# Optimization experiments

Hardware: AMD Instinct MI355X
Metric: run time of the kernel (lower is better)

The kernel has to match this reference:

```python
import jax, jax.numpy as jnp
import numpy as np

B, S, IN, OUT, L, R = 2, 8192, 2048, 2048, 4, 32


def setup_inputs() -> dict:
    key = jax.random.key(0)
    ks = jax.random.split(key, 6)
    return {
        "x": jax.random.normal(ks[0], (B, S, IN), dtype=jnp.float32),
        "weight": jax.random.normal(ks[1], (OUT, IN), dtype=jnp.float32) * 0.02,
        "bias": jax.random.normal(ks[2], (OUT,), dtype=jnp.float32) * 0.02,
        "downs": jax.random.normal(ks[3], (L, R, IN), dtype=jnp.float32) * 0.02,
        "ups": jax.random.normal(ks[4], (L, OUT, R), dtype=jnp.float32) * 0.02,
        "scales": jax.random.uniform(ks[5], (L,), dtype=jnp.float32),
    }


def reference(x, weight, bias, downs, ups, scales):
    # Base linear: y = x @ W.T + b
    y = jnp.einsum("bsi,oi->bso", x, weight) + bias
    # Low-rank LoRA deltas, grouped across adapters:
    # tmp[b,s,l,r] = x @ down_l.T ; delta = sum_l scale_l * tmp_l @ up_l.T
    tmp = jnp.einsum("bsi,lri->bslr", x, downs)  # [B,S,L,R]
    tmp = tmp * scales[None, None, :, None]       # fold per-adapter scale
    delta = jnp.einsum("bslr,lor->bso", tmp, ups)  # [B,S,OUT]
    return y + delta
```

## Files before the change

kernel.cpp:

```cpp
#include <hip/hip_runtime.h>

#define M_DIM 16384
#define N_DIM 2048
#define K_DIM 2048
#define L_AD 4
#define R_AD 32

typedef __bf16 bf16_t;
typedef bf16_t bf16x8 __attribute__((ext_vector_type(8)));
typedef bf16_t bf16x4 __attribute__((ext_vector_type(4)));
typedef float f32x4 __attribute__((ext_vector_type(4)));

#define BM 128
#define BN 128
#define BK 64

__device__ __forceinline__ void async_load16(const void* g, void* l) {
  __builtin_amdgcn_global_load_lds(
      (const __attribute__((address_space(1))) unsigned int*)g,
      (__attribute__((address_space(3))) unsigned int*)l, 16, 0, 0);
}

__global__ __launch_bounds__(256) void convert_x_kernel(
    const float* __restrict__ X, bf16_t* __restrict__ Xb) {
  const size_t base = ((size_t)blockIdx.x * 256 + threadIdx.x) * 8;
  f32x4 lo = *(const f32x4*)(X + base);
  f32x4 hi = *(const f32x4*)(X + base + 4);
  bf16x8 v;
  v[0] = (bf16_t)lo[0]; v[1] = (bf16_t)lo[1];
  v[2] = (bf16_t)lo[2]; v[3] = (bf16_t)lo[3];
  v[4] = (bf16_t)hi[0]; v[5] = (bf16_t)hi[1];
  v[6] = (bf16_t)hi[2]; v[7] = (bf16_t)hi[3];
  *(bf16x8*)(Xb + base) = v;
}

__global__ __launch_bounds__(256) void build_weff_kernel(
    const float* __restrict__ W, const float* __restrict__ downs,
    const float* __restrict__ ups, const float* __restrict__ scales,
    bf16_t* __restrict__ weff) {
  __shared__ float up_s[64 * 129];
  __shared__ float down_s[128 * 64];
  const int t = threadIdx.x;
  const int n0 = blockIdx.y * 64;
  const int k0 = blockIdx.x * 64;

  for (int l = 0; l < L_AD; ++l) {
    const float sc = scales[l];
    const float* up_l = ups + (size_t)l * N_DIM * R_AD;
    #pragma unroll
    for (int j = 0; j < 8; ++j) {
      int flat = j * 256 + t;
      int nl = flat >> 5, r = flat & 31;
      up_s[nl * 129 + l * 32 + r] = sc * up_l[(size_t)(n0 + nl) * R_AD + r];
    }
  }
  #pragma unroll
  for (int j = 0; j < 32; ++j) {
    int flat = j * 256 + t;
    int lr = flat >> 6, kk = flat & 63;
    down_s[lr * 64 + kk] = downs[(size_t)lr * K_DIM + k0 + kk];
  }
  __syncthreads();

  const int tn = t >> 4, tk = t & 15;
  float acc[4][4] = {};
  for (int lr = 0; lr < L_AD * R_AD; ++lr) {
    f32x4 b = *(const f32x4*)&down_s[lr * 64 + tk * 4];
    #pragma unroll
    for (int u = 0; u < 4; ++u) {
      float a = up_s[(tn * 4 + u) * 129 + lr];
      #pragma unroll
      for (int v = 0; v < 4; ++v) acc[u][v] += a * b[v];
    }
  }
  #pragma unroll
  for (int u = 0; u < 4; ++u) {
    int n = n0 + tn * 4 + u;
    f32x4 wv = *(const f32x4*)&W[(size_t)n * K_DIM + k0 + tk * 4];
    bf16x4 o;
    #pragma unroll
    for (int v = 0; v < 4; ++v) o[v] = (bf16_t)(acc[u][v] + wv[v]);
    *(bf16x4*)&weff[(size_t)n * K_DIM + k0 + tk * 4] = o;
  }
}

#define BARRIER() __builtin_amdgcn_s_barrier()
#define SCHEDB() __builtin_amdgcn_sched_barrier(0)
#define VMCNT4() asm volatile("s_waitcnt vmcnt(4)" ::: "memory")
#define VMCNT0() asm volatile("s_waitcnt vmcnt(0)" ::: "memory")

__global__ __launch_bounds__(512, 2) void gemm_bf16_256(
    const bf16_t* __restrict__ Xb, const bf16_t* __restrict__ Wb,
    const float* __restrict__ bias, float* __restrict__ out) {
  __shared__ __align__(16) bf16_t sm[2][2][16384];

  const int orig = blockIdx.x;
  const int swz = (orig & 7) * 64 + (orig >> 3);
  const int m0 = (swz >> 3) * 256;
  const int n0 = (swz & 7) * 256;

  const int t = threadIdx.x;
  const int l = t & 63;
  const int w = t >> 6;
  const int wm = w >> 2, wn = w & 3;
  const int col = l & 15, quad = l >> 4;

  const int d0 = w * 64 + l;
  const int row0 = d0 >> 3;
  const int c0 = (d0 & 7) ^ (row0 & 7);
  const bf16_t* Ab = Xb + (size_t)(m0 + row0) * K_DIM + c0 * 8;
  const bf16_t* Bb = Wb + (size_t)(n0 + row0) * K_DIM + c0 * 8;

  const int arow = wm * 128 + col;
  const int brow = wn * 64 + col;

  float bn[4];
  #pragma unroll
  for (int g = 0; g < 4; ++g) bn[g] = bias[n0 + wn * 64 + g * 16 + col];

  f32x4 acc[8][4] = {};
  bf16x8 aLo[4][2], aHi[4][2], bB[4][2];

#define STG(Gb, B_, OP, H, KT)                                                 \
  do {                                                                         \
    async_load16((Gb) + ((size_t)(H)*128) * K_DIM + (size_t)(KT)*64,           \
                 &sm[B_][OP][(H)*8192 + d0 * 8]);                              \
    async_load16((Gb) + ((size_t)(H)*128 + 64) * K_DIM + (size_t)(KT)*64,      \
                 &sm[B_][OP][(H)*8192 + (d0 + 512) * 8]);                      \
  } while (0)

#define RDA(dst, fi, F0, B_)                                                   \
  do {                                                                         \
    const int R_ = arow + ((F0) + (fi)) * 16;                                  \
    const int rl_ = R_ & 127, h_ = R_ >> 7;                                    \
    _Pragma("unroll") for (int ks_ = 0; ks_ < 2; ++ks_) {                      \
      const int sl_ = (ks_ * 4 + quad) ^ (rl_ & 7);                            \
      dst[fi][ks_] =                                                           \
          *(const bf16x8*)&sm[B_][0][h_ * 8192 + (rl_ * 8 + sl_) * 8];         \
    }                                                                          \
  } while (0)

#define RDB(gi, B_)                                                            \
  do {                                                                         \
    const int R_ = brow + (gi) * 16;                                           \
    const int rl_ = R_ & 127, h_ = R_ >> 7;                                    \
    _Pragma("unroll") for (int ks_ = 0; ks_ < 2; ++ks_) {                      \
      const int sl_ = (ks_ * 4 + quad) ^ (rl_ & 7);                            \
      bB[gi][ks_] =                                                            \
          *(const bf16x8*)&sm[B_][1][h_ * 8192 + (rl_ * 8 + sl_) * 8];         \
    }                                                                          \
  } while (0)

#define MF(AARR, FA, G0)                                                       \
  do {                                                                         \
    __builtin_amdgcn_s_setprio(1);                                             \
    _Pragma("unroll") for (int f_ = 0; f_ < 4; ++f_)                           \
        _Pragma("unroll") for (int g_ = 0; g_ < 2; ++g_)                       \
            _Pragma("unroll") for (int ks_ = 0; ks_ < 2; ++ks_)                \
                acc[(FA) + f_][(G0) + g_] =                                    \
                    __builtin_amdgcn_mfma_f32_16x16x32_bf16(                   \
                        AARR[f_][ks_], bB[(G0) + g_][ks_],                     \
                        acc[(FA) + f_][(G0) + g_], 0, 0, 0);                   \
    __builtin_amdgcn_s_setprio(0);                                             \
  } while (0)

  STG(Bb, 0, 1, 0, 0); STG(Bb, 0, 1, 1, 0);
  STG(Ab, 0, 0, 0, 0); STG(Ab, 0, 0, 1, 0);
  STG(Bb, 1, 1, 0, 1); STG(Bb, 1, 1, 1, 1);
  VMCNT4();
  BARRIER();

  for (int j = 0; j < 16; ++j) {
    const int k1 = 2 * j + 1;
    const int kt2 = (2 * j + 2 < 32) ? 2 * j + 2 : 31;
    const int kt3 = (2 * j + 3 < 32) ? 2 * j + 3 : 31;

    STG(Ab, 1, 0, 0, k1); SCHEDB();
    RDA(aLo, 0, 0, 0); RDB(0, 0); RDB(1, 0);
    RDA(aLo, 1, 0, 0); RDA(aLo, 2, 0, 0); RDA(aLo, 3, 0, 0);
    SCHEDB();
    RDB(2, 0); RDB(3, 0);
    SCHEDB();
    MF(aLo, 0, 0);
    SCHEDB(); BARRIER();
    STG(Ab, 1, 0, 1, k1); SCHEDB();
    RDA(aHi, 0, 4, 0); RDA(aHi, 1, 4, 0); RDA(aHi, 2, 4, 0); RDA(aHi, 3, 4, 0);
    SCHEDB();
    MF(aLo, 0, 2);
    SCHEDB(); BARRIER();
    STG(Bb, 0, 1, 0, kt2); SCHEDB();
    MF(aHi, 4, 2);
    SCHEDB(); BARRIER();
    STG(Bb, 0, 1, 1, kt2); SCHEDB();
    MF(aHi, 4, 0);
    SCHEDB(); VMCNT4(); BARRIER();
    STG(Ab, 0, 0, 0, kt2); SCHEDB();
    RDA(aLo, 0, 0, 1); RDB(0, 1); RDB(1, 1);
    RDA(aLo, 1, 0, 1); RDA(aLo, 2, 0, 1); RDA(aLo, 3, 0, 1);
    SCHEDB();
    RDB(2, 1); RDB(3, 1);
    SCHEDB();
    MF(aLo, 0, 0);
    SCHEDB(); BARRIER();
    STG(Ab, 0, 0, 1, kt2); SCHEDB();
    RDA(aHi, 0, 4, 1); RDA(aHi, 1, 4, 1); RDA(aHi, 2, 4, 1); RDA(aHi, 3, 4, 1);
    SCHEDB();
    MF(aLo, 0, 2);
    SCHEDB(); BARRIER();
    STG(Bb, 1, 1, 0, kt3); SCHEDB();
    MF(aHi, 4, 2);
    SCHEDB(); BARRIER();
    STG(Bb, 1, 1, 1, kt3); SCHEDB();
    MF(aHi, 4, 0);
    SCHEDB(); VMCNT4(); BARRIER();
  }

  VMCNT0();
  BARRIER();

  #pragma unroll
  for (int f = 0; f < 8; ++f) {
    const int m = m0 + wm * 128 + f * 16 + quad * 4;
    const bf16x8* dummy = 0; (void)dummy;
    #pragma unroll
    for (int g = 0; g < 4; ++g) {
      const int n = n0 + wn * 64 + g * 16 + col;
      float* op = out + (size_t)m * N_DIM + n;
      #pragma unroll
      for (int r = 0; r < 4; ++r) op[(size_t)r * N_DIM] = acc[f][g][r] + bn[g];
    }
  }
#undef STG
#undef RDA
#undef RDB
#undef MF
}

#define SA 72
__global__ __launch_bounds__(256) void lora_gemm_fallback(
    const float* __restrict__ X, const bf16_t* __restrict__ Wb,
    const float* __restrict__ bias, float* __restrict__ out) {
  __shared__ __align__(16) bf16_t As[BM * SA];
  __shared__ __align__(16) bf16_t Bs[BN * BK];

  const int t = threadIdx.x;
  const int lane = t & 63;
  const int wv = t >> 6;
  const int wm = wv >> 1, wn = wv & 1;
  const int col = lane & 15, quad = lane >> 4;
  const int m0 = blockIdx.y * BM;
  const int n0 = blockIdx.x * BN;
  const int srow = t >> 3;
  const int soct = t & 7;

  f32x4 acc[4][4] = {};
  float bn[4];
  #pragma unroll
  for (int j = 0; j < 4; ++j) bn[j] = bias[n0 + wn * 64 + j * 16 + col];

  for (int kt = 0; kt < K_DIM / BK; ++kt) {
    const int kg = kt * BK;
    #pragma unroll
    for (int j = 0; j < 4; ++j) {
      int n = j * 32 + srow;
      int c = soct ^ (n & 7);
      async_load16(Wb + (size_t)(n0 + n) * K_DIM + kg + c * 8,
                   &Bs[(size_t)(j * 256 + t) * 8]);
    }
    #pragma unroll
    for (int j = 0; j < 4; ++j) {
      int m = j * 32 + srow;
      const f32x4* src = (const f32x4*)(X + (size_t)(m0 + m) * K_DIM + kg + soct * 8);
      f32x4 lo = src[0], hi = src[1];
      bf16x8 v;
      v[0] = (bf16_t)lo[0]; v[1] = (bf16_t)lo[1];
      v[2] = (bf16_t)lo[2]; v[3] = (bf16_t)lo[3];
      v[4] = (bf16_t)hi[0]; v[5] = (bf16_t)hi[1];
      v[6] = (bf16_t)hi[2]; v[7] = (bf16_t)hi[3];
      *(bf16x8*)&As[m * SA + soct * 8] = v;
    }
    __syncthreads();

    #pragma unroll
    for (int ks = 0; ks < 2; ++ks) {
      bf16x8 af[4], bfr[4];
      #pragma unroll
      for (int i = 0; i < 4; ++i)
        af[i] = *(const bf16x8*)&As[(wm * 64 + i * 16 + col) * SA + ks * 32 + quad * 8];
      #pragma unroll
      for (int j = 0; j < 4; ++j) {
        int n = wn * 64 + j * 16 + col;
        int p = (ks * 4 + quad) ^ (n & 7);
        bfr[j] = *(const bf16x8*)&Bs[n * BK + p * 8];
      }
      #pragma unroll
      for (int i = 0; i < 4; ++i) {
        #pragma unroll
        for (int j = 0; j < 4; ++j)
          acc[i][j] = __builtin_amdgcn_mfma_f32_16x16x32_bf16(af[i], bfr[j], acc[i][j], 0, 0, 0);
      }
    }
    __syncthreads();
  }

  #pragma unroll
  for (int i = 0; i < 4; ++i) {
    #pragma unroll
    for (int r = 0; r < 4; ++r) {
      int m = m0 + wm * 64 + i * 16 + quad * 4 + r;
      float* orow = out + (size_t)m * N_DIM + n0 + wn * 64 + col;
      #pragma unroll
      for (int j = 0; j < 4; ++j)
        orow[j * 16] = acc[i][j][r] + bn[j];
    }
  }
}

extern "C" void kernel_launch(void* const* d_in, const int* in_sizes, int n_in,
                              void* d_out, int out_size, void* d_ws, size_t ws_size,
                              hipStream_t stream) {
  const float* x      = (const float*)d_in[0];
  const float* weight = (const float*)d_in[1];
  const float* bias   = (const float*)d_in[2];
  const float* downs  = (const float*)d_in[3];
  const float* ups    = (const float*)d_in[4];
  const float* scales = (const float*)d_in[5];
  float* out = (float*)d_out;

  const size_t weff_bytes = (size_t)N_DIM * K_DIM * 2;
  const size_t xb_bytes   = (size_t)M_DIM * K_DIM * 2;
  bf16_t* weff = (bf16_t*)d_ws;

  dim3 g1(K_DIM / 64, N_DIM / 64);
  build_weff_kernel<<<g1, 256, 0, stream>>>(weight, downs, ups, scales, weff);

  if (ws_size >= weff_bytes + xb_bytes) {
    bf16_t* xb = (bf16_t*)((char*)d_ws + weff_bytes);
    const size_t n_elem = (size_t)M_DIM * K_DIM;
    convert_x_kernel<<<(unsigned)(n_elem / (256 * 8)), 256, 0, stream>>>(x, xb);
    gemm_bf16_256<<<dim3((M_DIM / 256) * (N_DIM / 256)), 512, 0, stream>>>(
        xb, weff, bias, out);
  } else {
    dim3 g2(N_DIM / BN, M_DIM / BM);
    lora_gemm_fallback<<<g2, 256, 0, stream>>>(x, weff, bias, out);
  }
}
```

Before: 370.5 us.

## Switch main GEMM to 32x32x16 MFMA with fine-grained lgkmcnt-pipelined phases

Replaces the 16x16x32 bf16 MFMA tiling with 32x32x16 MFMAs, so each wave computes a 128x64 tile as 4x2 blocks of 32x32. LDS fragment reads and their lane mapping are reworked to match. The main loop is split into phases that issue LDS reads, then stage the next global-to-LDS copy, then interleave MFMAs with partial lgkmcnt waits so compute can start before every fragment has arrived. Larger MFMAs need fewer instructions and fewer LDS reads per flop. The costs are a more complex hand schedule with more barriers and a different register footprint.

```diff
diff --git a/kernel.cpp b/kernel.cpp
--- a/kernel.cpp
+++ b/kernel.cpp
@@ -10,6 +10,7 @@
 typedef bf16_t bf16x8 __attribute__((ext_vector_type(8)));
 typedef bf16_t bf16x4 __attribute__((ext_vector_type(4)));
 typedef float f32x4 __attribute__((ext_vector_type(4)));
+typedef float f32x16 __attribute__((ext_vector_type(16)));
 
 #define BM 128
 #define BN 128
@@ -86,6 +87,7 @@
 
 #define BARRIER() __builtin_amdgcn_s_barrier()
 #define SCHEDB() __builtin_amdgcn_sched_barrier(0)
+#define LGKM(N) asm volatile("s_waitcnt lgkmcnt(" #N ")" ::: "memory")
 #define VMCNT4() asm volatile("s_waitcnt vmcnt(4)" ::: "memory")
 #define VMCNT0() asm volatile("s_waitcnt vmcnt(0)" ::: "memory")
 
@@ -103,7 +105,8 @@
   const int l = t & 63;
   const int w = t >> 6;
   const int wm = w >> 2, wn = w & 3;
-  const int col = l & 15, quad = l >> 4;
+  const int l5 = l & 31;
+  const int half = l >> 5;
 
   const int d0 = w * 64 + l;
   const int row0 = d0 >> 3;
@@ -111,15 +114,12 @@
   const bf16_t* Ab = Xb + (size_t)(m0 + row0) * K_DIM + c0 * 8;
   const bf16_t* Bb = Wb + (size_t)(n0 + row0) * K_DIM + c0 * 8;
 
-  const int arow = wm * 128 + col;
-  const int brow = wn * 64 + col;
-
-  float bn[4];
-  #pragma unroll
-  for (int g = 0; g < 4; ++g) bn[g] = bias[n0 + wn * 64 + g * 16 + col];
-
-  f32x4 acc[8][4] = {};
-  bf16x8 aLo[4][2], aHi[4][2], bB[4][2];
+  float bn[2];
+  #pragma unroll
+  for (int g = 0; g < 2; ++g) bn[g] = bias[n0 + wn * 64 + g * 32 + l5];
+
+  f32x16 acc[4][2] = {};
+  bf16x8 aLo[2][4], aHi[2][4], bB[2][4];
 
 #define STG(Gb, B_, OP, H, KT)                                                 \
   do {                                                                         \
@@ -129,39 +129,27 @@
                  &sm[B_][OP][(H)*8192 + (d0 + 512) * 8]);                      \
   } while (0)
 
-#define RDA(dst, fi, F0, B_)                                                   \
+#define RA(dst, fi, F, ks, B_)                                                 \
   do {                                                                         \
-    const int R_ = arow + ((F0) + (fi)) * 16;                                  \
+    const int rl_ = (F)*32 + l5;                                               \
+    const int sl_ = ((ks)*2 + half) ^ (rl_ & 7);                               \
+    dst[fi][ks] = *(const bf16x8*)&sm[B_][0][wm * 8192 + (rl_ * 8 + sl_) * 8]; \
+  } while (0)
+
+#define RB(gi, ks, B_)                                                         \
+  do {                                                                         \
+    const int R_ = wn * 64 + (gi)*32 + l5;                                     \
     const int rl_ = R_ & 127, h_ = R_ >> 7;                                    \
-    _Pragma("unroll") for (int ks_ = 0; ks_ < 2; ++ks_) {                      \
-      const int sl_ = (ks_ * 4 + quad) ^ (rl_ & 7);                            \
-      dst[fi][ks_] =                                                           \
-          *(const bf16x8*)&sm[B_][0][h_ * 8192 + (rl_ * 8 + sl_) * 8];         \
-    }                                                                          \
+    const int sl_ = ((ks)*2 + half) ^ (rl_ & 7);                               \
+    bB[gi][ks] = *(const bf16x8*)&sm[B_][1][h_ * 8192 + (rl_ * 8 + sl_) * 8];  \
   } while (0)
 
-#define RDB(gi, B_)                                                            \
+#define MF2(AARR, FA, G, ks)                                                   \
   do {                                                                         \
-    const int R_ = brow + (gi) * 16;                                           \
-    const int rl_ = R_ & 127, h_ = R_ >> 7;                                    \
-    _Pragma("unroll") for (int ks_ = 0; ks_ < 2; ++ks_) {                      \
-      const int sl_ = (ks_ * 4 + quad) ^ (rl_ & 7);                            \
-      bB[gi][ks_] =                                                            \
-          *(const bf16x8*)&sm[B_][1][h_ * 8192 + (rl_ * 8 + sl_) * 8];         \
-    }                                                                          \
-  } while (0)
-
-#define MF(AARR, FA, G0)                                                       \
-  do {                                                                         \
-    __builtin_amdgcn_s_setprio(1);                                             \
-    _Pragma("unroll") for (int f_ = 0; f_ < 4; ++f_)                           \
-        _Pragma("unroll") for (int g_ = 0; g_ < 2; ++g_)                       \
-            _Pragma("unroll") for (int ks_ = 0; ks_ < 2; ++ks_)                \
-                acc[(FA) + f_][(G0) + g_] =                                    \
-                    __builtin_amdgcn_mfma_f32_16x16x32_bf16(                   \
-                        AARR[f_][ks_], bB[(G0) + g_][ks_],                     \
-                        acc[(FA) + f_][(G0) + g_], 0, 0, 0);                   \
-    __builtin_amdgcn_s_setprio(0);                                             \
+    acc[(FA) + 0][G] = __builtin_amdgcn_mfma_f32_32x32x16_bf16(                \
+        AARR[0][ks], bB[G][ks], acc[(FA) + 0][G], 0, 0, 0);                    \
+    acc[(FA) + 1][G] = __builtin_amdgcn_mfma_f32_32x32x16_bf16(                \
+        AARR[1][ks], bB[G][ks], acc[(FA) + 1][G], 0, 0, 0);                    \
   } while (0)
 
   STG(Bb, 0, 1, 0, 0); STG(Bb, 0, 1, 1, 0);
@@ -175,65 +163,94 @@
     const int kt2 = (2 * j + 2 < 32) ? 2 * j + 2 : 31;
     const int kt3 = (2 * j + 3 < 32) ? 2 * j + 3 : 31;
 
-    STG(Ab, 1, 0, 0, k1); SCHEDB();
-    RDA(aLo, 0, 0, 0); RDB(0, 0); RDB(1, 0);
-    RDA(aLo, 1, 0, 0); RDA(aLo, 2, 0, 0); RDA(aLo, 3, 0, 0);
-    SCHEDB();
-    RDB(2, 0); RDB(3, 0);
-    SCHEDB();
-    MF(aLo, 0, 0);
+#define PH_A_LO_B0(B_, SGB, SGOP, SGH, SGK)                                    \
+                \
+    RA(aLo, 0, 0, 0, B_); RA(aLo, 1, 1, 0, B_); RB(0, 0, B_);                  \
+    RA(aLo, 0, 0, 1, B_); RA(aLo, 1, 1, 1, B_); RB(0, 1, B_);                  \
+    RA(aLo, 0, 0, 2, B_); RA(aLo, 1, 1, 2, B_); RB(0, 2, B_);                  \
+    RA(aLo, 0, 0, 3, B_); RA(aLo, 1, 1, 3, B_); RB(0, 3, B_);                  \
+    STG(SGB, SGOP, SGH, SGK >> 16, SGK & 0xffff);                              \
+    SCHEDB(); BARRIER();                                                       \
+    __builtin_amdgcn_s_setprio(1);                                             \
+    LGKM(9); SCHEDB(); MF2(aLo, 0, 0, 0);                                      \
+    LGKM(6); SCHEDB(); MF2(aLo, 0, 0, 1);                                      \
+    LGKM(3); SCHEDB(); MF2(aLo, 0, 0, 2);                                      \
+    LGKM(0); SCHEDB(); MF2(aLo, 0, 0, 3);                                      \
+    __builtin_amdgcn_s_setprio(0);                                             \
     SCHEDB(); BARRIER();
-    STG(Ab, 1, 0, 1, k1); SCHEDB();
-    RDA(aHi, 0, 4, 0); RDA(aHi, 1, 4, 0); RDA(aHi, 2, 4, 0); RDA(aHi, 3, 4, 0);
-    SCHEDB();
-    MF(aLo, 0, 2);
+
+#define PH_B1(B_, SGB, SGOP, SGH, SGK)                                         \
+                                           \
+    RB(1, 0, B_); RB(1, 1, B_); RB(1, 2, B_); RB(1, 3, B_);                    \
+    STG(SGB, SGOP, SGH, SGK >> 16, SGK & 0xffff);                              \
+    SCHEDB(); BARRIER();                                                       \
+    __builtin_amdgcn_s_setprio(1);                                             \
+    LGKM(3); SCHEDB(); MF2(aLo, 0, 1, 0);                                      \
+    LGKM(2); SCHEDB(); MF2(aLo, 0, 1, 1);                                      \
+    LGKM(1); SCHEDB(); MF2(aLo, 0, 1, 2);                                      \
+    LGKM(0); SCHEDB(); MF2(aLo, 0, 1, 3);                                      \
+    __builtin_amdgcn_s_setprio(0);                                             \
     SCHEDB(); BARRIER();
-    STG(Bb, 0, 1, 0, kt2); SCHEDB();
-    MF(aHi, 4, 2);
+
+#define PH_A_HI(B_, SGB, SGOP, SGH, SGK)                                       \
+                                     \
+    RA(aHi, 0, 2, 0, B_); RA(aHi, 1, 3, 0, B_);                                \
+    RA(aHi, 0, 2, 1, B_); RA(aHi, 1, 3, 1, B_);                                \
+    RA(aHi, 0, 2, 2, B_); RA(aHi, 1, 3, 2, B_);                                \
+    RA(aHi, 0, 2, 3, B_); RA(aHi, 1, 3, 3, B_);                                \
+    STG(SGB, SGOP, SGH, SGK >> 16, SGK & 0xffff);                              \
+    SCHEDB(); BARRIER();                                                       \
+    __builtin_amdgcn_s_setprio(1);                                             \
+    LGKM(6); SCHEDB(); MF2(aHi, 2, 1, 0);                                      \
+    LGKM(4); SCHEDB(); MF2(aHi, 2, 1, 1);                                      \
+    LGKM(2); SCHEDB(); MF2(aHi, 2, 1, 2);                                      \
+    LGKM(0); SCHEDB(); MF2(aHi, 2, 1, 3);                                      \
+    __builtin_amdgcn_s_setprio(0);                                             \
     SCHEDB(); BARRIER();
-    STG(Bb, 0, 1, 1, kt2); SCHEDB();
-    MF(aHi, 4, 0);
+
+#define PH_LAST(SGB, SGOP, SGH, SGK)                                           \
+                               \
+    STG(SGB, SGOP, SGH, SGK >> 16, SGK & 0xffff);                              \
+    SCHEDB(); BARRIER(); SCHEDB();                                             \
+    __builtin_amdgcn_s_setprio(1);                                             \
+    MF2(aHi, 2, 0, 0); MF2(aHi, 2, 0, 1);                                      \
+    MF2(aHi, 2, 0, 2); MF2(aHi, 2, 0, 3);                                      \
+    __builtin_amdgcn_s_setprio(0);                                             \
     SCHEDB(); VMCNT4(); BARRIER();
-    STG(Ab, 0, 0, 0, kt2); SCHEDB();
-    RDA(aLo, 0, 0, 1); RDB(0, 1); RDB(1, 1);
-    RDA(aLo, 1, 0, 1); RDA(aLo, 2, 0, 1); RDA(aLo, 3, 0, 1);
-    SCHEDB();
-    RDB(2, 1); RDB(3, 1);
-    SCHEDB();
-    MF(aLo, 0, 0);
-    SCHEDB(); BARRIER();
-    STG(Ab, 0, 0, 1, kt2); SCHEDB();
-    RDA(aHi, 0, 4, 1); RDA(aHi, 1, 4, 1); RDA(aHi, 2, 4, 1); RDA(aHi, 3, 4, 1);
-    SCHEDB();
-    MF(aLo, 0, 2);
-    SCHEDB(); BARRIER();
-    STG(Bb, 1, 1, 0, kt3); SCHEDB();
-    MF(aHi, 4, 2);
-    SCHEDB(); BARRIER();
-    STG(Bb, 1, 1, 1, kt3); SCHEDB();
-    MF(aHi, 4, 0);
-    SCHEDB(); VMCNT4(); BARRIER();
+
+    PH_A_LO_B0(0, Ab, 1, 0, ((0 << 16) | k1))
+    PH_B1    (0, Ab, 1, 0, ((1 << 16) | k1))
+    PH_A_HI  (0, Bb, 0, 1, ((0 << 16) | kt2))
+    PH_LAST  (   Bb, 0, 1, ((1 << 16) | kt2))
+    PH_A_LO_B0(1, Ab, 0, 0, ((0 << 16) | kt2))
+    PH_B1    (1, Ab, 0, 0, ((1 << 16) | kt2))
+    PH_A_HI  (1, Bb, 1, 1, ((0 << 16) | kt3))
+    PH_LAST  (   Bb, 1, 1, ((1 << 16) | kt3))
   }
 
   VMCNT0();
   BARRIER();
 
   #pragma unroll
-  for (int f = 0; f < 8; ++f) {
-    const int m = m0 + wm * 128 + f * 16 + quad * 4;
-    const bf16x8* dummy = 0; (void)dummy;
-    #pragma unroll
-    for (int g = 0; g < 4; ++g) {
-      const int n = n0 + wn * 64 + g * 16 + col;
-      float* op = out + (size_t)m * N_DIM + n;
-      #pragma unroll
-      for (int r = 0; r < 4; ++r) op[(size_t)r * N_DIM] = acc[f][g][r] + bn[g];
+  for (int f = 0; f < 4; ++f) {
+    #pragma unroll
+    for (int g = 0; g < 2; ++g) {
+      const int n = n0 + wn * 64 + g * 32 + l5;
+      #pragma unroll
+      for (int r = 0; r < 16; ++r) {
+        const int m = m0 + wm * 128 + f * 32 + (r & 3) + 8 * (r >> 2) + 4 * half;
+        out[(size_t)m * N_DIM + n] = acc[f][g][r] + bn[g];
+      }
     }
   }
 #undef STG
-#undef RDA
-#undef RDB
-#undef MF
+#undef RA
+#undef RB
+#undef MF2
+#undef PH_A_LO_B0
+#undef PH_B1
+#undef PH_A_HI
+#undef PH_LAST
 }
 
 #define SA 72
```

Result: slower. 385.9 us (+4.2%).
